# Kernel tuning notes

Measured on AMD Instinct MI355X. Metric: run time of the kernel, lower is better.

Reference implementation:

```python
import jax, jax.numpy as jnp
import numpy as np

HEAD_DIM = 64
EMBED_DIM = 1024

def setup_inputs() -> dict:
    key = jax.random.key(0)
    k1, k2, k3, k4 = jax.random.split(key, 4)
    x = jax.random.normal(k1, (4, 4096, EMBED_DIM), dtype=jnp.float32)
    # nn.Linear(embed_dim, head_dim, bias=False): weight shape (head_dim, embed_dim)
    s = 1.0 / np.sqrt(EMBED_DIM)
    Wq = jax.random.uniform(k2, (HEAD_DIM, EMBED_DIM), jnp.float32, -s, s)
    Wk = jax.random.uniform(k3, (HEAD_DIM, EMBED_DIM), jnp.float32, -s, s)
    Wv = jax.random.uniform(k4, (HEAD_DIM, EMBED_DIM), jnp.float32, -s, s)
    return {"x": x, "Wq": Wq, "Wk": Wk, "Wv": Wv}

def reference(x, Wq, Wk, Wv):
    # Faithful to source: V = self.key(x), i.e. uses Wk (Wv is an unused param).
    n_ctx = x.shape[1]
    Q = jnp.einsum('bse,de->bsd', x, Wq)
    K = jnp.einsum('bse,de->bsd', x, Wk)
    V = jnp.einsum('bse,de->bsd', x, Wk)
    scale = 1.0 / jnp.sqrt(jnp.asarray(K.shape[-1], x.dtype))
    scores = jnp.einsum('bqd,bkd->bqk', Q, K) * scale  # [b, n_ctx, n_ctx]
    causal = jnp.tril(jnp.ones((n_ctx, n_ctx), dtype=bool))
    scores = jnp.where(causal, scores, jnp.asarray(-jnp.inf, scores.dtype))
    attn = jax.nn.softmax(scores, axis=-1)
    # dropout(p=0.2) omitted: reference runs in eval mode (identity)
    out = jnp.einsum('bqk,bkd->bqd', attn, V)
    return out
```

## Files before the change

kernel.cpp:

```cpp
#include <hip/hip_runtime.h>

typedef _Float16 f16;
typedef _Float16 f16x8 __attribute__((ext_vector_type(8)));
typedef _Float16 f16x4 __attribute__((ext_vector_type(4)));
typedef float f32x4 __attribute__((ext_vector_type(4)));

#define S_LEN 4096
#define B_SZ  4
#define E_DIM 1024
#define D_DIM 64
#define NROWS (B_SZ * S_LEN)
#define QSCALE (0.125f * 1.44269504088896f)
#define SMAX 8.0f

__device__ __forceinline__ float exp2g(float x) { return __builtin_amdgcn_exp2f(x); }

__global__ __launch_bounds__(256) void wpack_kernel(const float* __restrict__ Wq,
                                                    const float* __restrict__ Wk,
                                                    f16* __restrict__ Bp) {
    int id = blockIdx.x * 256 + threadIdx.x;
    int lane = id & 63, kc = (id >> 6) & 31, n = id >> 11;
    int row = n * 16 + (lane & 15);
    int col = kc * 32 + (lane >> 4) * 8;
    const float* src = (row < 64) ? (Wq + (long)row * E_DIM + col)
                                  : (Wk + (long)(row - 64) * E_DIM + col);
    float4 v0 = ((const float4*)src)[0];
    float4 v1 = ((const float4*)src)[1];
    f16x8 h = {(f16)v0.x, (f16)v0.y, (f16)v0.z, (f16)v0.w,
               (f16)v1.x, (f16)v1.y, (f16)v1.z, (f16)v1.w};
    *(f16x8*)(Bp + (long)id * 8) = h;
}

__global__ __launch_bounds__(256, 4) void proj_kernel(const float* __restrict__ x,
                                                      const f16* __restrict__ Bp,
                                                      f16* __restrict__ Qh,
                                                      f16* __restrict__ Kh) {
    __shared__ union {
        f16   xs[16][1040];
        float rb[4][16][132];
    } sm;

    const int tid  = threadIdx.x;
    const int w    = tid >> 6;
    const int lane = tid & 63;
    const int l15  = lane & 15;
    const int quad = lane >> 4;
    const long m0  = (long)blockIdx.x * 16;

#pragma unroll
    for (int c = 0; c < 16; c++) {
        int f4 = c * 256 + tid;
        int row = f4 >> 8;
        int col = (f4 & 255) * 4;
        float4 v = *(const float4*)(x + (m0 + row) * E_DIM + col);
        f16x4 h = {(f16)v.x, (f16)v.y, (f16)v.z, (f16)v.w};
        *(f16x4*)&sm.xs[row][col] = h;
    }
    __syncthreads();

    f32x4 acc[8];
#pragma unroll
    for (int n = 0; n < 8; n++) acc[n] = (f32x4){0.f, 0.f, 0.f, 0.f};

    const int kc0 = w * 8;
#pragma unroll
    for (int s = 0; s < 8; s++) {
        f16x8 a = *(const f16x8*)&sm.xs[l15][w * 256 + s * 32 + quad * 8];
#pragma unroll
        for (int n = 0; n < 8; n++) {
            f16x8 b = *(const f16x8*)(Bp + (((long)n * 32 + kc0 + s) * 64 + lane) * 8);
            acc[n] = __builtin_amdgcn_mfma_f32_16x16x32_f16(a, b, acc[n], 0, 0, 0);
        }
    }
    __syncthreads();

#pragma unroll
    for (int n = 0; n < 8; n++)
#pragma unroll
        for (int r = 0; r < 4; r++)
            sm.rb[w][quad * 4 + r][n * 16 + l15] = acc[n][r];
    __syncthreads();

    const int row = tid >> 4;
    const int c0  = (tid & 15) * 8;
    float sum[8];
#pragma unroll
    for (int i = 0; i < 8; i++) sum[i] = 0.f;
#pragma unroll
    for (int w4 = 0; w4 < 4; w4++)
#pragma unroll
        for (int g = 0; g < 2; g++) {
            f32x4 u = *(const f32x4*)&sm.rb[w4][row][c0 + g * 4];
#pragma unroll
            for (int i = 0; i < 4; i++) sum[g * 4 + i] += u[i];
        }

    const long grow = m0 + row;
    f16 tmp[8];
    if (c0 < 64) {
#pragma unroll
        for (int i = 0; i < 8; i++) tmp[i] = (f16)(sum[i] * QSCALE);
        *(f16x8*)(Qh + grow * 64 + c0) = *(f16x8*)tmp;
    } else {
#pragma unroll
        for (int i = 0; i < 8; i++) tmp[i] = (f16)sum[i];
        *(f16x8*)(Kh + grow * 64 + (c0 - 64)) = *(f16x8*)tmp;
    }
}

__global__ __launch_bounds__(256) void kpack_kernel(const f16* __restrict__ Kh,
                                                    f16* __restrict__ Khp,
                                                    f16* __restrict__ Kvp) {
    __shared__ __align__(16) f16 T[64][72];
    const int tid  = threadIdx.x;
    const int lane = tid & 63;
    const int l15  = lane & 15;
    const int quad = lane >> 4;
    const int g    = tid >> 6;
    const int b    = blockIdx.x >> 6;
    const int c    = blockIdx.x & 63;
    const f16* src = Kh + ((long)b * S_LEN + c * 64) * 64;
    const long chunk = (long)b * 64 + c;

    {
        int s = tid >> 2;
        int col = (tid & 3) * 16;
        f16x8 v0 = *(const f16x8*)(src + s * 64 + col);
        f16x8 v1 = *(const f16x8*)(src + s * 64 + col + 8);
        *(f16x8*)&T[s][col]     = v0;
        *(f16x8*)&T[s][col + 8] = v1;
    }
    __syncthreads();

    const int t = g;
    {
#pragma unroll
        for (int kf = 0; kf < 2; kf++) {
            f16x8 v = *(const f16x8*)&T[t * 16 + l15][kf * 32 + quad * 8];
            *(f16x8*)(Khp + chunk * 4096 + (t * 2 + kf) * 512 + lane * 8) = v;
        }
    }
    {
        f16 tmp[16];
#pragma unroll
        for (int n = 0; n < 4; n++)
#pragma unroll
            for (int j = 0; j < 4; j++)
                tmp[n * 4 + j] = T[t * 16 + quad * 4 + j][n * 16 + l15];
        f16* dst = Kvp + chunk * 4096 + t * 1024 + lane * 16;
        *(f16x8*)dst       = *(f16x8*)&tmp[0];
        *(f16x8*)(dst + 8) = *(f16x8*)&tmp[8];
    }
}

__global__ __launch_bounds__(256, 2) void attn_kernel(const f16* __restrict__ Qh,
                                                      const f16* __restrict__ Khp,
                                                      const f16* __restrict__ Kvp,
                                                      float* __restrict__ Out) {
    __shared__ float Ro[4][32][68];
    __shared__ float Rl[4][32];

    const int tid  = threadIdx.x;
    const int w    = tid >> 6;
    const int lane = tid & 63;
    const int l15  = lane & 15;
    const int quad = lane >> 4;

    const int bid  = blockIdx.x;
    const int q32  = 127 - (bid >> 2);
    const int b    = bid & 3;
    const int q0   = q32 * 32;
    const int jmax = q32 >> 1;

    const f16* Qb = Qh + (long)b * S_LEN * 64;
    f16x8 Aq[2][2];
#pragma unroll
    for (int g = 0; g < 2; g++)
#pragma unroll
        for (int kf = 0; kf < 2; kf++)
            Aq[g][kf] = *(const f16x8*)(Qb + (long)(q0 + g * 16 + l15) * 64 + kf * 32 + quad * 8);

    const f16x4 ones = {(f16)1.f, (f16)1.f, (f16)1.f, (f16)1.f};
    f32x4 O[2][4];
    f32x4 Lacc[2];
#pragma unroll
    for (int g = 0; g < 2; g++) {
        Lacc[g] = (f32x4){0.f, 0.f, 0.f, 0.f};
#pragma unroll
        for (int n = 0; n < 4; n++) O[g][n] = (f32x4){0.f, 0.f, 0.f, 0.f};
    }

    const long cb = (long)b * 64;

#define LOADKA(buf, jj)                                                        \
    {                                                                          \
        const f16* p_ = Khp + (cb + (jj)) * 4096 + lane * 8;                   \
        _Pragma("unroll")                                                      \
        for (int q8 = 0; q8 < 8; q8++) buf[q8] = *(const f16x8*)(p_ + q8 * 512);\
    }

#define COMPUTE(buf, jj)                                                       \
    {                                                                          \
        const f16* kv_ = Kvp + (cb + (jj)) * 4096 + lane * 16;                 \
        const int tlim = ((jj) == jmax) ? (((q0 + 31 - jmax * 64) >> 4) + 1) : 4; \
        _Pragma("unroll")                                                      \
        for (int t = 0; t < 4; t++) {                                          \
            if (t < tlim) {                                                    \
                f32x4 St0 = (f32x4){0.f, 0.f, 0.f, 0.f};                       \
                f32x4 St1 = (f32x4){0.f, 0.f, 0.f, 0.f};                       \
                St0 = __builtin_amdgcn_mfma_f32_16x16x32_f16(buf[t * 2],     Aq[0][0], St0, 0, 0, 0); \
                St0 = __builtin_amdgcn_mfma_f32_16x16x32_f16(buf[t * 2 + 1], Aq[0][1], St0, 0, 0, 0); \
                St1 = __builtin_amdgcn_mfma_f32_16x16x32_f16(buf[t * 2],     Aq[1][0], St1, 0, 0, 0); \
                St1 = __builtin_amdgcn_mfma_f32_16x16x32_f16(buf[t * 2 + 1], Aq[1][1], St1, 0, 0, 0); \
                if ((jj) == jmax) {                                            \
                    int kc_ = jmax * 64 + t * 16 + quad * 4;                   \
                    _Pragma("unroll")                                          \
                    for (int r = 0; r < 4; r++) {                              \
                        if (kc_ + r > q0 + l15)      St0[r] = -1e30f;          \
                        if (kc_ + r > q0 + 16 + l15) St1[r] = -1e30f;          \
                    }                                                          \
                }                                                              \
                f16x4 P0, P1;                                                  \
                _Pragma("unroll")                                              \
                for (int r = 0; r < 4; r++) {                                  \
                    P0[r] = (f16)exp2g(St0[r] - SMAX);                         \
                    P1[r] = (f16)exp2g(St1[r] - SMAX);                         \
                }                                                              \
                Lacc[0] = __builtin_amdgcn_mfma_f32_16x16x16f16(P0, ones, Lacc[0], 0, 0, 0); \
                Lacc[1] = __builtin_amdgcn_mfma_f32_16x16x16f16(P1, ones, Lacc[1], 0, 0, 0); \
                f16x8 v0 = *(const f16x8*)(kv_ + t * 1024);                    \
                f16x8 v1 = *(const f16x8*)(kv_ + t * 1024 + 8);                \
                f16x4 b0 = __builtin_shufflevector(v0, v0, 0, 1, 2, 3);        \
                f16x4 b1 = __builtin_shufflevector(v0, v0, 4, 5, 6, 7);        \
                f16x4 b2 = __builtin_shufflevector(v1, v1, 0, 1, 2, 3);        \
                f16x4 b3 = __builtin_shufflevector(v1, v1, 4, 5, 6, 7);        \
                O[0][0] = __builtin_amdgcn_mfma_f32_16x16x16f16(P0, b0, O[0][0], 0, 0, 0); \
                O[0][1] = __builtin_amdgcn_mfma_f32_16x16x16f16(P0, b1, O[0][1], 0, 0, 0); \
                O[0][2] = __builtin_amdgcn_mfma_f32_16x16x16f16(P0, b2, O[0][2], 0, 0, 0); \
                O[0][3] = __builtin_amdgcn_mfma_f32_16x16x16f16(P0, b3, O[0][3], 0, 0, 0); \
                O[1][0] = __builtin_amdgcn_mfma_f32_16x16x16f16(P1, b0, O[1][0], 0, 0, 0); \
                O[1][1] = __builtin_amdgcn_mfma_f32_16x16x16f16(P1, b1, O[1][1], 0, 0, 0); \
                O[1][2] = __builtin_amdgcn_mfma_f32_16x16x16f16(P1, b2, O[1][2], 0, 0, 0); \
                O[1][3] = __builtin_amdgcn_mfma_f32_16x16x16f16(P1, b3, O[1][3], 0, 0, 0); \
            }                                                                  \
        }                                                                      \
    }

    f16x8 kaA[8], kaB[8];
    int j = w;
    if (j <= jmax) LOADKA(kaA, j);
    while (j <= jmax) {
        if (j + 4 <= jmax) LOADKA(kaB, j + 4);
        COMPUTE(kaA, j);
        j += 4;
        if (j > jmax) break;
        if (j + 4 <= jmax) LOADKA(kaA, j + 4);
        COMPUTE(kaB, j);
        j += 4;
    }
#undef LOADKA
#undef COMPUTE

#pragma unroll
    for (int g = 0; g < 2; g++) {
#pragma unroll
        for (int n = 0; n < 4; n++)
#pragma unroll
            for (int r = 0; r < 4; r++)
                Ro[w][g * 16 + quad * 4 + r][n * 16 + l15] = O[g][n][r];
        if (l15 == 0)
#pragma unroll
            for (int r = 0; r < 4; r++)
                Rl[w][g * 16 + quad * 4 + r] = Lacc[g][r];
    }
    __syncthreads();

    const int row = tid >> 3;
    const int c0  = (tid & 7) * 8;
    float sum[8];
#pragma unroll
    for (int i = 0; i < 8; i++) sum[i] = 0.f;
    float lt = 0.f;
#pragma unroll
    for (int w4 = 0; w4 < 4; w4++) {
        lt += Rl[w4][row];
#pragma unroll
        for (int g4 = 0; g4 < 2; g4++) {
            f32x4 u = *(const f32x4*)&Ro[w4][row][c0 + g4 * 4];
#pragma unroll
            for (int i = 0; i < 4; i++) sum[g4 * 4 + i] += u[i];
        }
    }
    float inv = 1.0f / lt;
    float* dst = Out + ((long)b * S_LEN + q0 + row) * 64 + c0;
    *(float4*)dst       = make_float4(sum[0] * inv, sum[1] * inv, sum[2] * inv, sum[3] * inv);
    *(float4*)(dst + 4) = make_float4(sum[4] * inv, sum[5] * inv, sum[6] * inv, sum[7] * inv);
}

extern "C" void kernel_launch(void* const* d_in, const int* in_sizes, int n_in,
                              void* d_out, int out_size, void* d_ws, size_t ws_size,
                              hipStream_t stream) {
    const float* x  = (const float*)d_in[0];
    const float* Wq = (const float*)d_in[1];
    const float* Wk = (const float*)d_in[2];
    float* out = (float*)d_out;

    f16* Qh  = (f16*)d_ws;
    f16* Kh  = Qh + (long)NROWS * D_DIM;
    f16* Bp  = Kh + (long)NROWS * D_DIM;
    f16* Khp = Bp + (long)128 * E_DIM;
    f16* Kvp = Khp + (long)NROWS * D_DIM;

    wpack_kernel<<<dim3(64), dim3(256), 0, stream>>>(Wq, Wk, Bp);
    proj_kernel<<<dim3(NROWS / 16), dim3(256), 0, stream>>>(x, Bp, Qh, Kh);
    kpack_kernel<<<dim3(B_SZ * 64), dim3(256), 0, stream>>>(Kh, Khp, Kvp);
    attn_kernel<<<dim3(B_SZ * 128), dim3(256), 0, stream>>>(Qh, Khp, Kvp, out);
}
```

Measured before the change: 144.1 us.

## Fuse K packing into projection with double-buffered x tiles and reorder attention blocks

```diff
diff --git a/kernel.cpp b/kernel.cpp
--- a/kernel.cpp
+++ b/kernel.cpp
@@ -31,125 +31,120 @@
     *(f16x8*)(Bp + (long)id * 8) = h;
 }
 
-__global__ __launch_bounds__(256, 4) void proj_kernel(const float* __restrict__ x,
+__global__ __launch_bounds__(512, 2) void proj_kernel(const float* __restrict__ x,
                                                       const f16* __restrict__ Bp,
                                                       f16* __restrict__ Qh,
-                                                      f16* __restrict__ Kh) {
+                                                      f16* __restrict__ Khp,
+                                                      f16* __restrict__ Kvp) {
     __shared__ union {
-        f16   xs[16][1040];
-        float rb[4][16][132];
+        float xs[2][64][68];
+        float ro[8][16][68];
     } sm;
 
     const int tid  = threadIdx.x;
-    const int w    = tid >> 6;
+    const int wav  = tid >> 6;
+    const int w_m  = wav >> 1;
+    const int w_n  = wav & 1;
     const int lane = tid & 63;
     const int l15  = lane & 15;
     const int quad = lane >> 4;
-    const long m0  = (long)blockIdx.x * 16;
-
-#pragma unroll
+    const long m0  = (long)blockIdx.x * 64;
+
+    f32x4 acc[4];
+#pragma unroll
+    for (int n = 0; n < 4; n++) acc[n] = (f32x4){0.f, 0.f, 0.f, 0.f};
+
+    float4 ra[2];
+    const int r0[2]  = { (tid * 2 + 0) >> 4,  (tid * 2 + 1) >> 4 };
+    (void)r0;
+
+#pragma unroll
+    for (int j = 0; j < 2; j++) {
+        int idx = j * 512 + tid;
+        int row = idx >> 4, c4 = idx & 15;
+        ra[j] = *(const float4*)(x + (m0 + row) * E_DIM + c4 * 4);
+    }
+#pragma unroll
+    for (int j = 0; j < 2; j++) {
+        int idx = j * 512 + tid;
+        int row = idx >> 4, c4 = idx & 15;
+        *(f32x4*)&sm.xs[0][row][c4 * 4] = (f32x4){ra[j].x, ra[j].y, ra[j].z, ra[j].w};
+    }
+    __syncthreads();
+
     for (int c = 0; c < 16; c++) {
-        int f4 = c * 256 + tid;
-        int row = f4 >> 8;
-        int col = (f4 & 255) * 4;
-        float4 v = *(const float4*)(x + (m0 + row) * E_DIM + col);
-        f16x4 h = {(f16)v.x, (f16)v.y, (f16)v.z, (f16)v.w};
-        *(f16x4*)&sm.xs[row][col] = h;
-    }
+        const int cur = c & 1;
+        if (c + 1 < 16) {
+#pragma unroll
+            for (int j = 0; j < 2; j++) {
+                int idx = j * 512 + tid;
+                int row = idx >> 4, c4 = idx & 15;
+                ra[j] = *(const float4*)(x + (m0 + row) * E_DIM + (c + 1) * 64 + c4 * 4);
+            }
+        }
+#pragma unroll
+        for (int kf = 0; kf < 2; kf++) {
+            f32x4 a0 = *(const f32x4*)&sm.xs[cur][w_m * 16 + l15][kf * 32 + quad * 8];
+            f32x4 a1 = *(const f32x4*)&sm.xs[cur][w_m * 16 + l15][kf * 32 + quad * 8 + 4];
+            f16x8 A = {(f16)a0[0], (f16)a0[1], (f16)a0[2], (f16)a0[3],
+                       (f16)a1[0], (f16)a1[1], (f16)a1[2], (f16)a1[3]};
+            const int kc = c * 2 + kf;
+#pragma unroll
+            for (int nn = 0; nn < 4; nn++) {
+                const int n = w_n * 4 + nn;
+                f16x8 B = *(const f16x8*)(Bp + (((long)n * 32 + kc) * 64 + lane) * 8);
+                acc[nn] = __builtin_amdgcn_mfma_f32_16x16x32_f16(A, B, acc[nn], 0, 0, 0);
+            }
+        }
+        if (c + 1 < 16) {
+#pragma unroll
+            for (int j = 0; j < 2; j++) {
+                int idx = j * 512 + tid;
+                int row = idx >> 4, c4 = idx & 15;
+                *(f32x4*)&sm.xs[cur ^ 1][row][c4 * 4] = (f32x4){ra[j].x, ra[j].y, ra[j].z, ra[j].w};
+            }
+        }
+        __syncthreads();
+    }
+
+    const int s = wav;
+#pragma unroll
+    for (int nn = 0; nn < 4; nn++)
+#pragma unroll
+        for (int r = 0; r < 4; r++)
+            sm.ro[s][quad * 4 + r][nn * 16 + l15] = acc[nn][r];
     __syncthreads();
 
-    f32x4 acc[8];
-#pragma unroll
-    for (int n = 0; n < 8; n++) acc[n] = (f32x4){0.f, 0.f, 0.f, 0.f};
-
-    const int kc0 = w * 8;
-#pragma unroll
-    for (int s = 0; s < 8; s++) {
-        f16x8 a = *(const f16x8*)&sm.xs[l15][w * 256 + s * 32 + quad * 8];
-#pragma unroll
-        for (int n = 0; n < 8; n++) {
-            f16x8 b = *(const f16x8*)(Bp + (((long)n * 32 + kc0 + s) * 64 + lane) * 8);
-            acc[n] = __builtin_amdgcn_mfma_f32_16x16x32_f16(a, b, acc[n], 0, 0, 0);
-        }
-    }
-    __syncthreads();
-
-#pragma unroll
-    for (int n = 0; n < 8; n++)
-#pragma unroll
-        for (int r = 0; r < 4; r++)
-            sm.rb[w][quad * 4 + r][n * 16 + l15] = acc[n][r];
-    __syncthreads();
-
-    const int row = tid >> 4;
-    const int c0  = (tid & 15) * 8;
-    float sum[8];
-#pragma unroll
-    for (int i = 0; i < 8; i++) sum[i] = 0.f;
-#pragma unroll
-    for (int w4 = 0; w4 < 4; w4++)
-#pragma unroll
-        for (int g = 0; g < 2; g++) {
-            f32x4 u = *(const f32x4*)&sm.rb[w4][row][c0 + g * 4];
-#pragma unroll
-            for (int i = 0; i < 4; i++) sum[g * 4 + i] += u[i];
-        }
-
-    const long grow = m0 + row;
-    f16 tmp[8];
-    if (c0 < 64) {
-#pragma unroll
-        for (int i = 0; i < 8; i++) tmp[i] = (f16)(sum[i] * QSCALE);
-        *(f16x8*)(Qh + grow * 64 + c0) = *(f16x8*)tmp;
+    if (w_n == 0) {
+        float q[16];
+#pragma unroll
+        for (int g = 0; g < 4; g++)
+            *(f32x4*)&q[g * 4] = *(const f32x4*)&sm.ro[s][l15][quad * 16 + g * 4];
+        f16 o[16];
+#pragma unroll
+        for (int i = 0; i < 16; i++) o[i] = (f16)(q[i] * QSCALE);
+        f16* dst = Qh + (m0 + w_m * 16 + l15) * 64 + quad * 16;
+        *(f16x8*)dst       = *(f16x8*)&o[0];
+        *(f16x8*)(dst + 8) = *(f16x8*)&o[8];
     } else {
-#pragma unroll
-        for (int i = 0; i < 8; i++) tmp[i] = (f16)sum[i];
-        *(f16x8*)(Kh + grow * 64 + (c0 - 64)) = *(f16x8*)tmp;
-    }
-}
-
-__global__ __launch_bounds__(256) void kpack_kernel(const f16* __restrict__ Kh,
-                                                    f16* __restrict__ Khp,
-                                                    f16* __restrict__ Kvp) {
-    __shared__ __align__(16) f16 T[64][72];
-    const int tid  = threadIdx.x;
-    const int lane = tid & 63;
-    const int l15  = lane & 15;
-    const int quad = lane >> 4;
-    const int g    = tid >> 6;
-    const int b    = blockIdx.x >> 6;
-    const int c    = blockIdx.x & 63;
-    const f16* src = Kh + ((long)b * S_LEN + c * 64) * 64;
-    const long chunk = (long)b * 64 + c;
-
-    {
-        int s = tid >> 2;
-        int col = (tid & 3) * 16;
-        f16x8 v0 = *(const f16x8*)(src + s * 64 + col);
-        f16x8 v1 = *(const f16x8*)(src + s * 64 + col + 8);
-        *(f16x8*)&T[s][col]     = v0;
-        *(f16x8*)&T[s][col + 8] = v1;
-    }
-    __syncthreads();
-
-    const int t = g;
-    {
+        const long chunk = blockIdx.x;
 #pragma unroll
         for (int kf = 0; kf < 2; kf++) {
-            f16x8 v = *(const f16x8*)&T[t * 16 + l15][kf * 32 + quad * 8];
-            *(f16x8*)(Khp + chunk * 4096 + (t * 2 + kf) * 512 + lane * 8) = v;
-        }
-    }
-    {
-        f16 tmp[16];
-#pragma unroll
-        for (int n = 0; n < 4; n++)
+            f32x4 k0 = *(const f32x4*)&sm.ro[s][l15][kf * 32 + quad * 8];
+            f32x4 k1 = *(const f32x4*)&sm.ro[s][l15][kf * 32 + quad * 8 + 4];
+            f16x8 h = {(f16)k0[0], (f16)k0[1], (f16)k0[2], (f16)k0[3],
+                       (f16)k1[0], (f16)k1[1], (f16)k1[2], (f16)k1[3]};
+            *(f16x8*)(Khp + chunk * 4096 + (w_m * 2 + kf) * 512 + lane * 8) = h;
+        }
+        f16 t16[16];
+#pragma unroll
+        for (int nn = 0; nn < 4; nn++)
 #pragma unroll
             for (int j = 0; j < 4; j++)
-                tmp[n * 4 + j] = T[t * 16 + quad * 4 + j][n * 16 + l15];
-        f16* dst = Kvp + chunk * 4096 + t * 1024 + lane * 16;
-        *(f16x8*)dst       = *(f16x8*)&tmp[0];
-        *(f16x8*)(dst + 8) = *(f16x8*)&tmp[8];
+                t16[nn * 4 + j] = (f16)sm.ro[s][quad * 4 + j][nn * 16 + l15];
+        f16* dst = Kvp + chunk * 4096 + w_m * 1024 + lane * 16;
+        *(f16x8*)dst       = *(f16x8*)&t16[0];
+        *(f16x8*)(dst + 8) = *(f16x8*)&t16[8];
     }
 }
 
@@ -166,9 +161,10 @@
     const int l15  = lane & 15;
     const int quad = lane >> 4;
 
-    const int bid  = blockIdx.x;
-    const int q32  = 127 - (bid >> 2);
-    const int b    = bid & 3;
+    const int bid = blockIdx.x;
+    int q32, b;
+    if (bid < 256) { q32 = 127 - (bid >> 2); b = bid & 3; }
+    else           { int k = bid - 256; q32 = k >> 2; b = k & 3; }
     const int q0   = q32 * 32;
     const int jmax = q32 >> 1;
 
@@ -306,13 +302,11 @@
     float* out = (float*)d_out;
 
     f16* Qh  = (f16*)d_ws;
-    f16* Kh  = Qh + (long)NROWS * D_DIM;
-    f16* Bp  = Kh + (long)NROWS * D_DIM;
+    f16* Bp  = Qh + (long)NROWS * D_DIM;
     f16* Khp = Bp + (long)128 * E_DIM;
     f16* Kvp = Khp + (long)NROWS * D_DIM;
 
     wpack_kernel<<<dim3(64), dim3(256), 0, stream>>>(Wq, Wk, Bp);
-    proj_kernel<<<dim3(NROWS / 16), dim3(256), 0, stream>>>(x, Bp, Qh, Kh);
-    kpack_kernel<<<dim3(B_SZ * 64), dim3(256), 0, stream>>>(Kh, Khp, Kvp);
+    proj_kernel<<<dim3(NROWS / 64), dim3(512), 0, stream>>>(x, Bp, Qh, Khp, Kvp);
     attn_kernel<<<dim3(B_SZ * 128), dim3(256), 0, stream>>>(Qh, Khp, Kvp, out);
 }
```

Result: slower. 155.6 us (+8.0%).
